# Kernel optimization log

Hardware: AMD Instinct MI355X
Metric: run time of the kernel (lower is better)

## Reference

```python
import jax, jax.numpy as jnp
import numpy as np

N = 8192          # number of signals (rows of Y)
DIM_BASIS = 512   # signal dimension n
NUM_BASIS = 2048  # dictionary atoms m (overcomplete)
SC_ITERS = 20     # FISTA iterations
PM_ITERS = 100    # power-method iterations


def setup_inputs() -> dict:
    key = jax.random.key(0)
    kY, kW = jax.random.split(key)
    Y = jax.random.normal(kY, (N, DIM_BASIS), jnp.float32)
    W = jax.random.normal(kW, (DIM_BASIS, NUM_BASIS), jnp.float32)
    # NormDict applied in __init__: unit-norm columns
    W = W / jnp.linalg.norm(W, axis=0, keepdims=True)
    K = jnp.asarray(0.1, jnp.float32)  # lamda for FISTA soft-threshold
    return {"Y": Y, "W": W, "K": K}


def _soft(x, lam):
    return jnp.sign(x) * jax.nn.relu(jnp.abs(x) - lam)


def _power_method(W):
    # largest eigenvalue of W^T W (W: [n, m]); fixed random init for determinism
    X0 = jax.random.normal(jax.random.key(1), (1, W.shape[1]), W.dtype)

    def body(i, carry):
        X, _ = carry
        X = (X @ W.T) @ W          # X <- X W^T W, shape [1, m]
        nm = jnp.linalg.norm(X)
        return (X / nm, nm)

    _, nm = jax.lax.fori_loop(0, PM_ITERS, body, (X0, jnp.asarray(1.0, W.dtype)))
    return nm


def _fista(Y, W, lam, iters):
    c = _power_method(W)
    eta = 1.0 / c
    Gamma0 = _soft(Y @ (eta * W), lam)     # [N, m]
    Yn = jnp.linalg.norm(Y)

    def step(carry, _):
        Gamma, Z, t = carry
        residual = Z @ W.T - Y                              # [N, n]
        Gamma_new = _soft(Z - eta * (residual @ W), lam / c)
        t_new = (1.0 + jnp.sqrt(1.0 + 4.0 * t * t)) / 2.0
        Z_new = Gamma_new + ((t - 1.0) / t_new) * (Gamma_new - Gamma)
        nrm = jnp.linalg.norm(residual) / Yn
        return (Gamma_new, Z_new, t_new), nrm

    init = (Gamma0, Gamma0, jnp.asarray(1.0, Y.dtype))
    (Gamma, _, _), norms = jax.lax.scan(step, init, None, length=iters)
    return Gamma, norms


def reference(Y, W, K):
    # NormDict at start of forward (done on .data in torch -> no grad through norm)
    Wn = W / jax.lax.stop_gradient(jnp.linalg.norm(W, axis=0, keepdims=True))
    # W.requires_grad_(False) during sparse coding
    W_ng = jax.lax.stop_gradient(Wn)
    Gamma, norms = _fista(Y, W_ng, K, SC_ITERS)
    X = Gamma @ Wn.T   # reconstruction, grad flows to W here only
    return X, Gamma, norms
```

## Files before the change

kernel.cpp:

```cpp
#include <hip/hip_runtime.h>
#include <cmath>

#define NR   8192
#define DB   512
#define NB   2048
#define ITERS 20
#define NSQ   9

typedef _Float16 hfrag_t __attribute__((ext_vector_type(8)));
typedef __attribute__((ext_vector_type(4))) float accv_t;
typedef unsigned short us4 __attribute__((ext_vector_type(4)));
typedef unsigned short us8 __attribute__((ext_vector_type(8)));
typedef float f4 __attribute__((ext_vector_type(4)));

#define SL_Y2   0
#define SL_NUM  1
#define SL_DEN  2
#define SL_C    3
#define SL_ETA  4
#define SL_THR  5
#define SL_TR   6
#define SL_RES2 16

__device__ inline unsigned short f2h(float f) {
  _Float16 h = (_Float16)f;
  return __builtin_bit_cast(unsigned short, h);
}
__device__ inline float h2f(unsigned short u) {
  _Float16 h = __builtin_bit_cast(_Float16, u);
  return (float)h;
}
__device__ inline float softthr(float x, float t) {
  float a = fabsf(x) - t;
  return a > 0.f ? copysignf(a, x) : 0.f;
}


template<int MI, int NI, int NKT, int UNR>
__device__ inline void gemm_tt(const unsigned short* __restrict__ At, int NTka,
                               const unsigned short* __restrict__ Bt, int NTkb,
                               int mt0, int nt0, accv_t acc[MI][NI]) {
  const int lane = threadIdx.x & 63;
  const int l16 = lane & 15, quad = lane >> 4;
  const int off = l16 * 16 + (quad & 1) * 8;
  const int kh = quad >> 1;
#pragma unroll
  for (int mi = 0; mi < MI; ++mi)
#pragma unroll
    for (int ni = 0; ni < NI; ++ni) acc[mi][ni] = (accv_t){0.f, 0.f, 0.f, 0.f};

  auto kstep = [&](int kt) {
    const int ktile = (kt << 1) + kh;
    hfrag_t af[MI], bf[NI];
#pragma unroll
    for (int mi = 0; mi < MI; ++mi)
      af[mi] = *(const hfrag_t*)&At[(((size_t)(mt0 + mi) * NTka + ktile) << 8) + off];
#pragma unroll
    for (int ni = 0; ni < NI; ++ni)
      bf[ni] = *(const hfrag_t*)&Bt[(((size_t)(nt0 + ni) * NTkb + ktile) << 8) + off];
#pragma unroll
    for (int mi = 0; mi < MI; ++mi)
#pragma unroll
      for (int ni = 0; ni < NI; ++ni)
        acc[mi][ni] = __builtin_amdgcn_mfma_f32_16x16x32_f16(bf[ni], af[mi], acc[mi][ni], 0, 0, 0);
  };

  if constexpr (UNR == 8) {
#pragma unroll 8
    for (int kt = 0; kt < NKT; ++kt) kstep(kt);
  } else {
#pragma unroll 4
    for (int kt = 0; kt < NKT; ++kt) kstep(kt);
  }
}

__device__ inline size_t ctile_off(int mt, int nt, int NTn) {
  int lane = threadIdx.x & 63;
  return (((size_t)mt * NTn + nt) << 8) + (lane & 15) * 16 + (lane >> 4) * 4;
}

__global__ void k_zero(float* slots, float* colsq) {
  if (threadIdx.x < 64) slots[threadIdx.x] = 0.f;
  for (int i = threadIdx.x; i < NB; i += 256) colsq[i] = 0.f;
}

__global__ void k_colsq(const float* __restrict__ W, float* __restrict__ colsq) {
  int j = blockIdx.x * 256 + threadIdx.x;
  int r0 = blockIdx.y * 64;
  float s = 0.f;
  for (int i = 0; i < 64; ++i) { float v = W[(size_t)(r0 + i) * NB + j]; s += v * v; }
  atomicAdd(&colsq[j], s);
}

__global__ void k_wnorm(const float* __restrict__ W, const float* __restrict__ colsq,
                        unsigned short* __restrict__ Wn_t, unsigned short* __restrict__ Wt_t) {
  int tx = threadIdx.x & 31, ty = threadIdx.x >> 5;
  int j = blockIdx.x * 32 + tx;
  float inv = 1.0f / sqrtf(colsq[j]);
#pragma unroll
  for (int r = 0; r < 4; ++r) {
    int i = blockIdx.y * 32 + ty + r * 8;
    unsigned short h = f2h(W[(size_t)i * NB + j] * inv);
    Wn_t[(((size_t)(i >> 4) * (NB / 16) + (j >> 4)) << 8) + (i & 15) * 16 + (j & 15)] = h;
    Wt_t[(((size_t)(j >> 4) * (DB / 16) + (i >> 4)) << 8) + (j & 15) * 16 + (i & 15)] = h;
  }
}

__global__ __launch_bounds__(256) void k_ynorm(const float* __restrict__ Y,
                                               unsigned short* __restrict__ Yh,
                                               float* __restrict__ slots) {
  __shared__ float part[4];
  int w = threadIdx.x >> 6, lane = threadIdx.x & 63;
  float s = 0.f;
#pragma unroll
  for (int rr = 0; rr < 4; ++rr) {
    int m = blockIdx.x * 16 + w * 4 + rr;
    const float* yrow = &Y[(size_t)m * DB + lane * 8];
    f4 v0 = *(const f4*)yrow;
    f4 v1 = *(const f4*)(yrow + 4);
    us8 h;
#pragma unroll
    for (int q = 0; q < 4; ++q) {
      h[q] = f2h(v0[q]);     s += v0[q] * v0[q];
      h[4 + q] = f2h(v1[q]); s += v1[q] * v1[q];
    }
    *(us8*)&Yh[(((size_t)(m >> 4) * 32 + (lane >> 1)) << 8) + (m & 15) * 16 + (lane & 1) * 8] = h;
  }
  for (int off = 32; off > 0; off >>= 1) s += __shfl_xor(s, off);
  if (lane == 0) part[w] = s;
  __syncthreads();
  if (threadIdx.x == 0) atomicAdd(&slots[SL_Y2], part[0] + part[1] + part[2] + part[3]);
}

__global__ __launch_bounds__(256) void k_sq(const float* __restrict__ S, float* __restrict__ D,
                                            const float* __restrict__ trIn, float* __restrict__ trOut) {
  __shared__ float tA[32][33], tB[32][33];
  int tx = threadIdx.x & 31, ty = threadIdx.x >> 5;
  int r0 = blockIdx.y * 32, c0 = blockIdx.x * 32;
  float inv = 1.0f / trIn[0];
  float acc[4] = {0.f, 0.f, 0.f, 0.f};
  for (int kt = 0; kt < 16; ++kt) {
    __syncthreads();
#pragma unroll
    for (int r = 0; r < 4; ++r) {
      tA[ty + r * 8][tx] = S[(size_t)(r0 + ty + r * 8) * DB + kt * 32 + tx];
      tB[ty + r * 8][tx] = S[(size_t)(kt * 32 + ty + r * 8) * DB + c0 + tx];
    }
    __syncthreads();
#pragma unroll
    for (int kk = 0; kk < 32; ++kk) {
      float b = tB[kk][tx];
#pragma unroll
      for (int r = 0; r < 4; ++r) acc[r] += tA[ty + r * 8][kk] * b;
    }
  }
  float inv2 = inv * inv;
#pragma unroll
  for (int r = 0; r < 4; ++r) {
    int row = r0 + ty + r * 8, col = c0 + tx;
    float v = acc[r] * inv2;
    D[(size_t)row * DB + col] = v;
    if (row == col) atomicAdd(trOut, v);
  }
}

__global__ void k_rayleigh(const float* __restrict__ Bm, const float* __restrict__ S,
                           float* __restrict__ slots) {
  int tid = blockIdx.x * 256 + threadIdx.x;
  float num = 0.f, den = 0.f;
  for (int i = tid; i < DB * DB; i += 256 * 256) {
    float s = S[i];
    num += Bm[i] * s;
    if ((i >> 9) == (i & 511)) den += s;
  }
  for (int off = 32; off > 0; off >>= 1) { num += __shfl_xor(num, off); den += __shfl_xor(den, off); }
  if ((threadIdx.x & 63) == 0) { atomicAdd(&slots[SL_NUM], num); atomicAdd(&slots[SL_DEN], den); }
}

__global__ void k_derive(float* slots, const float* __restrict__ Kp) {
  if (threadIdx.x == 0) {
    float cc = slots[SL_NUM] / slots[SL_DEN];
    slots[SL_C] = cc;
    float eta = 1.0f / cc;
    slots[SL_ETA] = eta;
    slots[SL_THR] = Kp[0] * eta;
  }
}

__global__ void k_norms(const float* __restrict__ slots, float* __restrict__ out) {
  int i = threadIdx.x;
  if (i < ITERS) out[i] = sqrtf(slots[SL_RES2 + i] / slots[SL_Y2]);
}

__global__ __launch_bounds__(256, 1) void k_gemm_bbuild(const unsigned short* __restrict__ Wn_t,
                                                        float* __restrict__ Bm, float* __restrict__ slots) {
  accv_t acc[2][4];
  int w = threadIdx.x >> 6, lane = threadIdx.x & 63;
  int mt0 = blockIdx.y * 8 + w * 2, nt0 = blockIdx.x * 4;
  gemm_tt<2, 4, NB / 32, 8>(Wn_t, NB / 16, Wn_t, NB / 16, mt0, nt0, acc);
  int l16 = lane & 15, quad = lane >> 4;
  float tr = 0.f;
#pragma unroll
  for (int mi = 0; mi < 2; ++mi)
#pragma unroll
    for (int ni = 0; ni < 4; ++ni) {
      int m = (mt0 + mi) * 16 + l16, nb = (nt0 + ni) * 16 + quad * 4;
      *(f4*)&Bm[(size_t)m * DB + nb] = acc[mi][ni];
#pragma unroll
      for (int r = 0; r < 4; ++r)
        if (m == nb + r) tr += acc[mi][ni][r];
    }
  if (tr != 0.f) atomicAdd(&slots[SL_TR], tr);
}

__global__ __launch_bounds__(256) void k_gemm_init(const unsigned short* __restrict__ Yh,
                                                   const unsigned short* __restrict__ Wt_t,
                                                   const float* __restrict__ slots,
                                                   const float* __restrict__ Kp,
                                                   unsigned short* __restrict__ Gh,
                                                   unsigned short* __restrict__ Zh) {
  accv_t acc[4][4];
  int w = threadIdx.x >> 6;
  int h = blockIdx.x;
  int xcd = h & 7, slot = h >> 3;
  int band = xcd * 8 + (slot >> 4);
  int nt = slot & 15;
  int mt0 = band * 8 + (w >> 1) * 4, nt0 = nt * 8 + (w & 1) * 4;
  gemm_tt<4, 4, DB / 32, 4>(Yh, DB / 16, Wt_t, DB / 16, mt0, nt0, acc);
  float eta = slots[SL_ETA], lam = Kp[0];
#pragma unroll
  for (int mi = 0; mi < 4; ++mi)
#pragma unroll
    for (int ni = 0; ni < 4; ++ni) {
      size_t tb = ctile_off(mt0 + mi, nt0 + ni, NB / 16);
      us4 gq;
#pragma unroll
      for (int r = 0; r < 4; ++r) gq[r] = f2h(softthr(acc[mi][ni][r] * eta, lam));
      *(us4*)&Gh[tb] = gq;
      *(us4*)&Zh[tb] = gq;
    }
}

__global__ __launch_bounds__(256, 2) void k_gemm_res(const unsigned short* __restrict__ Zh,
                                                     const unsigned short* __restrict__ Wn_t,
                                                     const unsigned short* __restrict__ Yh,
                                                     unsigned short* __restrict__ Rh,
                                                     float* __restrict__ res2slot) {
  accv_t acc[2][4];
  int w = threadIdx.x >> 6;
  int h = blockIdx.x;
  int xcd = h & 7, slot = h >> 3;
  int band = xcd * 8 + (slot >> 3);
  int nt = slot & 7;
  int mt0 = band * 8 + w * 2, nt0 = nt * 4;
  gemm_tt<2, 4, NB / 32, 8>(Zh, NB / 16, Wn_t, NB / 16, mt0, nt0, acc);
  float s2 = 0.f;
#pragma unroll
  for (int mi = 0; mi < 2; ++mi)
#pragma unroll
    for (int ni = 0; ni < 4; ++ni) {
      size_t tb = ctile_off(mt0 + mi, nt0 + ni, DB / 16);
      us4 yq = *(const us4*)&Yh[tb];
      us4 rq;
#pragma unroll
      for (int r = 0; r < 4; ++r) {
        float rv = acc[mi][ni][r] - h2f(yq[r]);
        rq[r] = f2h(rv);
        s2 += rv * rv;
      }
      *(us4*)&Rh[tb] = rq;
    }
  for (int off = 32; off > 0; off >>= 1) s2 += __shfl_xor(s2, off);
  if ((threadIdx.x & 63) == 0) atomicAdd(res2slot, s2);
}

__global__ __launch_bounds__(256) void k_gemm_upd(const unsigned short* __restrict__ Rh,
                                                  const unsigned short* __restrict__ Wt_t,
                                                  const float* __restrict__ slots,
                                                  unsigned short* __restrict__ Gh,
                                                  unsigned short* __restrict__ Zh,
                                                  float* __restrict__ GammaOut,
                                                  float mom, int writeFinal) {
  accv_t acc[4][4];
  int w = threadIdx.x >> 6, lane = threadIdx.x & 63;
  int h = blockIdx.x;
  int xcd = h & 7, slot = h >> 3;
  int band = xcd * 8 + (slot >> 4);
  int nt = slot & 15;
  int mt0 = band * 8 + (w >> 1) * 4, nt0 = nt * 8 + (w & 1) * 4;
  gemm_tt<4, 4, DB / 32, 4>(Rh, DB / 16, Wt_t, DB / 16, mt0, nt0, acc);
  int l16 = lane & 15, quad = lane >> 4;
  float eta = slots[SL_ETA], thr = slots[SL_THR];
#pragma unroll
  for (int mi = 0; mi < 4; ++mi)
#pragma unroll
    for (int ni = 0; ni < 4; ++ni) {
      size_t tb = ctile_off(mt0 + mi, nt0 + ni, NB / 16);
      us4 zq = *(const us4*)&Zh[tb];
      us4 gq = *(const us4*)&Gh[tb];
      us4 gho, zho;
      f4 gf;
#pragma unroll
      for (int r = 0; r < 4; ++r) {
        float z = h2f(zq[r]);
        float gold = h2f(gq[r]);
        float gn = softthr(z - eta * acc[mi][ni][r], thr);
        float zn = gn + mom * (gn - gold);
        gho[r] = f2h(gn);
        zho[r] = f2h(zn);
        gf[r] = gn;
      }
      *(us4*)&Gh[tb] = gho;
      *(us4*)&Zh[tb] = zho;
      if (writeFinal) {
        int m = (mt0 + mi) * 16 + l16, nb = (nt0 + ni) * 16 + quad * 4;
        *(f4*)&GammaOut[(size_t)m * NB + nb] = gf;
      }
    }
}

__global__ __launch_bounds__(256, 2) void k_gemm_x(const unsigned short* __restrict__ Gh,
                                                   const unsigned short* __restrict__ Wn_t,
                                                   float* __restrict__ X) {
  accv_t acc[2][4];
  int w = threadIdx.x >> 6, lane = threadIdx.x & 63;
  int h = blockIdx.x;
  int xcd = h & 7, slot = h >> 3;
  int band = xcd * 8 + (slot >> 3);
  int nt = slot & 7;
  int mt0 = band * 8 + w * 2, nt0 = nt * 4;
  gemm_tt<2, 4, NB / 32, 8>(Gh, NB / 16, Wn_t, NB / 16, mt0, nt0, acc);
  int l16 = lane & 15, quad = lane >> 4;
#pragma unroll
  for (int mi = 0; mi < 2; ++mi)
#pragma unroll
    for (int ni = 0; ni < 4; ++ni) {
      int m = (mt0 + mi) * 16 + l16, nb = (nt0 + ni) * 16 + quad * 4;
      *(f4*)&X[(size_t)m * DB + nb] = acc[mi][ni];
    }
}

extern "C" void kernel_launch(void* const* d_in, const int* in_sizes, int n_in,
                              void* d_out, int out_size, void* d_ws, size_t ws_size,
                              hipStream_t stream) {
  const float* Y  = (const float*)d_in[0];
  const float* W  = (const float*)d_in[1];
  const float* Kp = (const float*)d_in[2];

  float* Xout     = (float*)d_out;
  float* GammaOut = Xout + (size_t)NR * DB;
  float* NormsOut = GammaOut + (size_t)NR * NB;

  char* p = (char*)d_ws;
  auto carve = [&](size_t bytes) -> void* {
    void* r = (void*)p; p += (bytes + 255) & ~(size_t)255; return r;
  };
  float* slots = (float*)carve(64 * 4);
  float* colsq = (float*)carve(NB * 4);
  float* Bmat  = (float*)carve((size_t)DB * DB * 4);
  float* S0    = (float*)carve((size_t)DB * DB * 4);
  float* S1    = (float*)carve((size_t)DB * DB * 4);
  unsigned short* Wn_t = (unsigned short*)carve((size_t)DB * NB * 2);
  unsigned short* Wt_t = (unsigned short*)carve((size_t)NB * DB * 2);
  unsigned short* Yh   = (unsigned short*)carve((size_t)NR * DB * 2);
  unsigned short* Rh   = (unsigned short*)carve((size_t)NR * DB * 2);
  unsigned short* Zh   = (unsigned short*)carve((size_t)NR * NB * 2);
  unsigned short* Gh   = (unsigned short*)carve((size_t)NR * NB * 2);

  k_zero<<<1, 256, 0, stream>>>(slots, colsq);
  k_colsq<<<dim3(NB / 256, DB / 64), 256, 0, stream>>>(W, colsq);
  k_wnorm<<<dim3(NB / 32, DB / 32), 256, 0, stream>>>(W, colsq, Wn_t, Wt_t);
  k_ynorm<<<512, 256, 0, stream>>>(Y, Yh, slots);

  k_gemm_bbuild<<<dim3(DB / 64, DB / 128), 256, 0, stream>>>(Wn_t, Bmat, slots);
  float* ss[2] = {S0, S1};
  for (int k = 0; k < NSQ; ++k) {
    const float* in = (k == 0) ? Bmat : ss[(k + 1) & 1];
    k_sq<<<dim3(16, 16), 256, 0, stream>>>(in, ss[k & 1], slots + SL_TR + k, slots + SL_TR + k + 1);
  }
  k_rayleigh<<<256, 256, 0, stream>>>(Bmat, ss[(NSQ + 1) & 1], slots);
  k_derive<<<1, 64, 0, stream>>>(slots, Kp);

  k_gemm_init<<<1024, 256, 0, stream>>>(Yh, Wt_t, slots, Kp, Gh, Zh);
  double t = 1.0;
  for (int i = 0; i < ITERS; ++i) {
    k_gemm_res<<<512, 256, 0, stream>>>(Zh, Wn_t, Yh, Rh, slots + SL_RES2 + i);
    double tn = (1.0 + sqrt(1.0 + 4.0 * t * t)) / 2.0;
    float mom = (float)((t - 1.0) / tn);
    t = tn;
    k_gemm_upd<<<1024, 256, 0, stream>>>(Rh, Wt_t, slots, Gh, Zh, GammaOut,
                                         mom, (i == ITERS - 1) ? 1 : 0);
  }
  k_gemm_x<<<512, 256, 0, stream>>>(Gh, Wn_t, Xout);
  k_norms<<<1, 64, 0, stream>>>(slots, NormsOut);
}
```

Baseline: 2.594 ms.

## Split-K the residual GEMM into two halves with a separate combine kernel

The residual GEMM (Z·Wᵀ, K=2048) is split into two K-halves run as 1024 blocks that write fp32 partials, and a new combine kernel then adds them, subtracts Y, writes the fp16 residual and accumulates its squared norm. This doubles the block count to fill more CUs, at the cost of an extra kernel launch and round-tripping two 16 MB fp32 partial buffers through memory every iteration. The GEMM helper also drops its unroll-8 variant in favour of a fixed unroll of 4, and the min-blocks hints in launch_bounds are removed from several kernels. Split-K only runs when the workspace is large enough, otherwise the old path is used.

```diff
diff --git a/kernel.cpp b/kernel.cpp
--- a/kernel.cpp
+++ b/kernel.cpp
@@ -36,7 +36,7 @@
 }
 
 
-template<int MI, int NI, int NKT, int UNR>
+template<int MI, int NI, int NKT>
 __device__ inline void gemm_tt(const unsigned short* __restrict__ At, int NTka,
                                const unsigned short* __restrict__ Bt, int NTkb,
                                int mt0, int nt0, accv_t acc[MI][NI]) {
@@ -49,7 +49,8 @@
 #pragma unroll
     for (int ni = 0; ni < NI; ++ni) acc[mi][ni] = (accv_t){0.f, 0.f, 0.f, 0.f};
 
-  auto kstep = [&](int kt) {
+#pragma unroll 4
+  for (int kt = 0; kt < NKT; ++kt) {
     const int ktile = (kt << 1) + kh;
     hfrag_t af[MI], bf[NI];
 #pragma unroll
@@ -63,14 +64,6 @@
 #pragma unroll
       for (int ni = 0; ni < NI; ++ni)
         acc[mi][ni] = __builtin_amdgcn_mfma_f32_16x16x32_f16(bf[ni], af[mi], acc[mi][ni], 0, 0, 0);
-  };
-
-  if constexpr (UNR == 8) {
-#pragma unroll 8
-    for (int kt = 0; kt < NKT; ++kt) kstep(kt);
-  } else {
-#pragma unroll 4
-    for (int kt = 0; kt < NKT; ++kt) kstep(kt);
   }
 }
 
@@ -192,12 +185,12 @@
   if (i < ITERS) out[i] = sqrtf(slots[SL_RES2 + i] / slots[SL_Y2]);
 }
 
-__global__ __launch_bounds__(256, 1) void k_gemm_bbuild(const unsigned short* __restrict__ Wn_t,
-                                                        float* __restrict__ Bm, float* __restrict__ slots) {
+__global__ __launch_bounds__(256) void k_gemm_bbuild(const unsigned short* __restrict__ Wn_t,
+                                                     float* __restrict__ Bm, float* __restrict__ slots) {
   accv_t acc[2][4];
   int w = threadIdx.x >> 6, lane = threadIdx.x & 63;
   int mt0 = blockIdx.y * 8 + w * 2, nt0 = blockIdx.x * 4;
-  gemm_tt<2, 4, NB / 32, 8>(Wn_t, NB / 16, Wn_t, NB / 16, mt0, nt0, acc);
+  gemm_tt<2, 4, NB / 32>(Wn_t, NB / 16, Wn_t, NB / 16, mt0, nt0, acc);
   int l16 = lane & 15, quad = lane >> 4;
   float tr = 0.f;
 #pragma unroll
@@ -226,7 +219,7 @@
   int band = xcd * 8 + (slot >> 4);
   int nt = slot & 15;
   int mt0 = band * 8 + (w >> 1) * 4, nt0 = nt * 8 + (w & 1) * 4;
-  gemm_tt<4, 4, DB / 32, 4>(Yh, DB / 16, Wt_t, DB / 16, mt0, nt0, acc);
+  gemm_tt<4, 4, DB / 32>(Yh, DB / 16, Wt_t, DB / 16, mt0, nt0, acc);
   float eta = slots[SL_ETA], lam = Kp[0];
 #pragma unroll
   for (int mi = 0; mi < 4; ++mi)
@@ -241,11 +234,60 @@
     }
 }
 
-__global__ __launch_bounds__(256, 2) void k_gemm_res(const unsigned short* __restrict__ Zh,
-                                                     const unsigned short* __restrict__ Wn_t,
-                                                     const unsigned short* __restrict__ Yh,
-                                                     unsigned short* __restrict__ Rh,
-                                                     float* __restrict__ res2slot) {
+__global__ __launch_bounds__(256) void k_gemm_res_part(const unsigned short* __restrict__ Zh,
+                                                       const unsigned short* __restrict__ Wn_t,
+                                                       float* __restrict__ P0,
+                                                       float* __restrict__ P1) {
+  accv_t acc[2][4];
+  int w = threadIdx.x >> 6;
+  int h = blockIdx.x;
+  int khalf = h >> 9;
+  int hh = h & 511;
+  int xcd = hh & 7, slot = hh >> 3;
+  int band = xcd * 8 + (slot >> 3);
+  int nt = slot & 7;
+  int mt0 = band * 8 + w * 2, nt0 = nt * 4;
+  const size_t koff = (size_t)khalf * 64 * 256;
+  gemm_tt<2, 4, NB / 64>(Zh + koff, NB / 16, Wn_t + koff, NB / 16, mt0, nt0, acc);
+  float* P = khalf ? P1 : P0;
+#pragma unroll
+  for (int mi = 0; mi < 2; ++mi)
+#pragma unroll
+    for (int ni = 0; ni < 4; ++ni) {
+      size_t tb = ctile_off(mt0 + mi, nt0 + ni, DB / 16);
+      *(f4*)&P[tb] = acc[mi][ni];
+    }
+}
+
+__global__ __launch_bounds__(256) void k_rescomb(const float* __restrict__ P0,
+                                                 const float* __restrict__ P1,
+                                                 const unsigned short* __restrict__ Yh,
+                                                 unsigned short* __restrict__ Rh,
+                                                 float* __restrict__ res2slot) {
+  float s2 = 0.f;
+  for (size_t u = (size_t)blockIdx.x * 256 + threadIdx.x; u < (size_t)(NR * DB / 4);
+       u += (size_t)gridDim.x * 256) {
+    f4 a = *(const f4*)&P0[u << 2];
+    f4 b = *(const f4*)&P1[u << 2];
+    us4 yq = *(const us4*)&Yh[u << 2];
+    us4 rq;
+#pragma unroll
+    for (int r = 0; r < 4; ++r) {
+      float rv = a[r] + b[r] - h2f(yq[r]);
+      rq[r] = f2h(rv);
+      s2 += rv * rv;
+    }
+    *(us4*)&Rh[u << 2] = rq;
+  }
+  for (int off = 32; off > 0; off >>= 1) s2 += __shfl_xor(s2, off);
+  if ((threadIdx.x & 63) == 0) atomicAdd(res2slot, s2);
+}
+
+__global__ __launch_bounds__(256) void k_gemm_res(const unsigned short* __restrict__ Zh,
+                                                  const unsigned short* __restrict__ Wn_t,
+                                                  const unsigned short* __restrict__ Yh,
+                                                  unsigned short* __restrict__ Rh,
+                                                  float* __restrict__ res2slot) {
   accv_t acc[2][4];
   int w = threadIdx.x >> 6;
   int h = blockIdx.x;
@@ -253,7 +295,7 @@
   int band = xcd * 8 + (slot >> 3);
   int nt = slot & 7;
   int mt0 = band * 8 + w * 2, nt0 = nt * 4;
-  gemm_tt<2, 4, NB / 32, 8>(Zh, NB / 16, Wn_t, NB / 16, mt0, nt0, acc);
+  gemm_tt<2, 4, NB / 32>(Zh, NB / 16, Wn_t, NB / 16, mt0, nt0, acc);
   float s2 = 0.f;
 #pragma unroll
   for (int mi = 0; mi < 2; ++mi)
@@ -288,7 +330,7 @@
   int band = xcd * 8 + (slot >> 4);
   int nt = slot & 15;
   int mt0 = band * 8 + (w >> 1) * 4, nt0 = nt * 8 + (w & 1) * 4;
-  gemm_tt<4, 4, DB / 32, 4>(Rh, DB / 16, Wt_t, DB / 16, mt0, nt0, acc);
+  gemm_tt<4, 4, DB / 32>(Rh, DB / 16, Wt_t, DB / 16, mt0, nt0, acc);
   int l16 = lane & 15, quad = lane >> 4;
   float eta = slots[SL_ETA], thr = slots[SL_THR];
 #pragma unroll
@@ -319,9 +361,9 @@
     }
 }
 
-__global__ __launch_bounds__(256, 2) void k_gemm_x(const unsigned short* __restrict__ Gh,
-                                                   const unsigned short* __restrict__ Wn_t,
-                                                   float* __restrict__ X) {
+__global__ __launch_bounds__(256) void k_gemm_x(const unsigned short* __restrict__ Gh,
+                                                const unsigned short* __restrict__ Wn_t,
+                                                float* __restrict__ X) {
   accv_t acc[2][4];
   int w = threadIdx.x >> 6, lane = threadIdx.x & 63;
   int h = blockIdx.x;
@@ -329,7 +371,7 @@
   int band = xcd * 8 + (slot >> 3);
   int nt = slot & 7;
   int mt0 = band * 8 + w * 2, nt0 = nt * 4;
-  gemm_tt<2, 4, NB / 32, 8>(Gh, NB / 16, Wn_t, NB / 16, mt0, nt0, acc);
+  gemm_tt<2, 4, NB / 32>(Gh, NB / 16, Wn_t, NB / 16, mt0, nt0, acc);
   int l16 = lane & 15, quad = lane >> 4;
 #pragma unroll
   for (int mi = 0; mi < 2; ++mi)
@@ -366,6 +408,9 @@
   unsigned short* Rh   = (unsigned short*)carve((size_t)NR * DB * 2);
   unsigned short* Zh   = (unsigned short*)carve((size_t)NR * NB * 2);
   unsigned short* Gh   = (unsigned short*)carve((size_t)NR * NB * 2);
+  float* P0 = (float*)carve((size_t)NR * DB * 4);
+  float* P1 = (float*)carve((size_t)NR * DB * 4);
+  const bool splitk = ((size_t)(p - (char*)d_ws) <= ws_size);
 
   k_zero<<<1, 256, 0, stream>>>(slots, colsq);
   k_colsq<<<dim3(NB / 256, DB / 64), 256, 0, stream>>>(W, colsq);
@@ -384,7 +429,12 @@
   k_gemm_init<<<1024, 256, 0, stream>>>(Yh, Wt_t, slots, Kp, Gh, Zh);
   double t = 1.0;
   for (int i = 0; i < ITERS; ++i) {
-    k_gemm_res<<<512, 256, 0, stream>>>(Zh, Wn_t, Yh, Rh, slots + SL_RES2 + i);
+    if (splitk) {
+      k_gemm_res_part<<<1024, 256, 0, stream>>>(Zh, Wn_t, P0, P1);
+      k_rescomb<<<1024, 256, 0, stream>>>(P0, P1, Yh, Rh, slots + SL_RES2 + i);
+    } else {
+      k_gemm_res<<<512, 256, 0, stream>>>(Zh, Wn_t, Yh, Rh, slots + SL_RES2 + i);
+    }
     double tn = (1.0 + sqrt(1.0 + 4.0 * t * t)) / 2.0;
     float mom = (float)((t - 1.0) / tn);
     t = tn;
```

Measured after the change: 3.315 ms. 27.8% more time.
